# Optimization experiments

Measured on AMD Instinct MI355X. Metric: run time of the kernel, lower is better.

## Reference

```python
import jax, jax.numpy as jnp
import numpy as np

INPUT_LEN = 100000
D_MODEL = 128
NUM_AREAS = 500
NUM_HEADS = 4
DEPTH = D_MODEL // NUM_HEADS          # 32
L = INPUT_LEN // NUM_AREAS            # 200 (per-area length)
MAX_LEN = 2 * (1 + L) - 1             # 401
MASK_NEG = float(np.finfo(np.float16).min) / 10.0  # -6553.6, as in source


def relative_shift(x):
    # x: [B, A, H, L, 2L-1] -> [B, A, H, L, L] (Transformer-XL shift trick)
    B, A, H, t1, m = x.shape
    x = jnp.pad(x, ((0, 0), (0, 0), (0, 0), (0, 0), (1, 0)))  # prepend zero col -> t2 = m+1 = 2L
    t2 = m + 1
    x = x.reshape(B, A, H, t2, t1)
    x = x[:, :, :, 1:, :]
    x = x.reshape(B, A, H, t1, t2 - 1)
    return x[..., : t2 // 2]


def setup_inputs() -> dict:
    key = jax.random.key(0)
    ks = jax.random.split(key, 9)
    s = 0.02
    inp = jax.random.normal(ks[0], (1, INPUT_LEN, D_MODEL), dtype=jnp.float32)
    mask = jax.random.bernoulli(ks[1], 0.1, (1, 1, 1, L, L)).astype(jnp.float32)
    Wq = jax.random.normal(ks[2], (D_MODEL, D_MODEL), dtype=jnp.float32) * s
    Wk = jax.random.normal(ks[3], (D_MODEL, D_MODEL), dtype=jnp.float32) * s
    Wv = jax.random.normal(ks[4], (D_MODEL, D_MODEL), dtype=jnp.float32) * s
    bq = jnp.zeros((D_MODEL,), jnp.float32)
    bk = jnp.zeros((D_MODEL,), jnp.float32)
    bv = jnp.zeros((D_MODEL,), jnp.float32)
    E = jax.random.normal(ks[5], (MAX_LEN, DEPTH), dtype=jnp.float32) * s
    return {"inp": inp, "mask": mask, "Wq": Wq, "bq": bq, "Wk": Wk, "bk": bk,
            "Wv": Wv, "bv": bv, "E": E}


def reference(inp, mask, Wq, bq, Wk, bk, Wv, bv, E):
    B = inp.shape[0]
    x = inp.reshape(B, NUM_AREAS, L, D_MODEL)  # split_areas

    def proj(W, b):
        y = jnp.einsum('bald,de->bale', x, W) + b
        return y.reshape(B, NUM_AREAS, L, NUM_HEADS, DEPTH).transpose(0, 1, 3, 2, 4)

    q = proj(Wq, bq)  # [B, A, H, L, depth]
    k = proj(Wk, bk)
    v = proj(Wv, bv)

    start = max(0, MAX_LEN - (2 * L - 1))  # static = 2
    Eu = E[start:]                          # [2L-1, depth]  (dropout is identity at inference)

    QE = jnp.einsum('bahld,md->bahlm', q, Eu)   # [B, A, H, L, 2L-1]
    Srel = relative_shift(QE)                   # [B, A, H, L, L]
    qk = jnp.einsum('bahld,bahmd->bahlm', q, k) # [B, A, H, L, L]
    logits = (qk + Srel) / jnp.sqrt(jnp.float32(D_MODEL))
    logits = logits + mask * jnp.float32(MASK_NEG)
    attn = jax.nn.softmax(logits, axis=-1)
    out = jnp.einsum('bahlm,bahmd->bahld', attn, v)   # [B, A, H, L, depth]
    out = out.transpose(0, 1, 3, 2, 4).reshape(B, NUM_AREAS, L, D_MODEL)
    return out, attn
```

## Files before the change

### kernel.cpp

```cpp
#include <hip/hip_runtime.h>

typedef short v8s __attribute__((ext_vector_type(8)));
typedef float v4f __attribute__((ext_vector_type(4)));

#define NBH      2000
#define LSEQ     200
#define LPAD     208
#define DEPTH    32
#define DMODEL   128
#define TEU      399
#define MASKNEG  (-6550.4f)
#define QSCALE   0.08838834764831845f

#define BH_ELE   (LPAD * DEPTH)
#define QW_OFF   0
#define KW_OFF   (NBH * BH_ELE)
#define VW_OFF   (2 * NBH * BH_ELE)
#define WT_OFF   (3 * NBH * BH_ELE)
#define EU_OFF   (WT_OFF + 3 * DMODEL * DMODEL)

__device__ __forceinline__ unsigned short f2b(float f) {
  unsigned u = __float_as_uint(f);
  unsigned r = 0x7fffu + ((u >> 16) & 1u);
  return (unsigned short)((u + r) >> 16);
}
__device__ __forceinline__ float b2f(unsigned short u) {
  return __uint_as_float(((unsigned)u) << 16);
}

__global__ void prep_kernel(const float* __restrict__ Wq, const float* __restrict__ Wk,
                            const float* __restrict__ Wv, const float* __restrict__ E,
                            unsigned short* __restrict__ ws) {
  unsigned short* WT = ws + WT_OFF;
  unsigned short* Eu = ws + EU_OFF;
  const int nW = 3 * DMODEL * DMODEL;
  const int total = nW + TEU * DEPTH;
  for (int i = blockIdx.x * blockDim.x + threadIdx.x; i < total; i += gridDim.x * blockDim.x) {
    if (i < nW) {
      int m = i >> 14; int r = i & 16383; int e = r >> 7; int kk = r & 127;
      const float* W = (m == 0) ? Wq : ((m == 1) ? Wk : Wv);
      WT[i] = f2b(W[kk * DMODEL + e]);
    } else {
      int j = i - nW;
      Eu[j] = f2b(E[2 * DEPTH + j]);
    }
  }
}

__global__ __launch_bounds__(256, 4)
void proj_kernel(const float* __restrict__ x, const float* __restrict__ bq,
                 const float* __restrict__ bk, const float* __restrict__ bv,
                 unsigned short* __restrict__ ws) {
  const unsigned short* WT = ws + WT_OFF;
  int bh = blockIdx.x; int a = bh >> 2; int h = bh & 3;
  int tid = threadIdx.x; int wave = tid >> 6; int lane = tid & 63;
  int g = lane >> 4; int c = lane & 15;

  for (int st = wave; st < 13; st += 4) {
    int l0 = st * 16;
    int row = a * LSEQ + min(l0 + c, LSEQ - 1);
    v8s afr[4];
#pragma unroll
    for (int ks = 0; ks < 4; ++ks) {
      const float* p = x + (size_t)row * DMODEL + ks * 32 + 8 * g;
      float4 f0 = *(const float4*)p;
      float4 f1 = *(const float4*)(p + 4);
      v8s t;
      t[0] = (short)f2b(f0.x); t[1] = (short)f2b(f0.y); t[2] = (short)f2b(f0.z); t[3] = (short)f2b(f0.w);
      t[4] = (short)f2b(f1.x); t[5] = (short)f2b(f1.y); t[6] = (short)f2b(f1.z); t[7] = (short)f2b(f1.w);
      afr[ks] = t;
    }
#pragma unroll
    for (int m = 0; m < 3; ++m) {
      const float* bp = (m == 0) ? bq : ((m == 1) ? bk : bv);
#pragma unroll
      for (int nt = 0; nt < 2; ++nt) {
        int col = h * DEPTH + nt * 16 + c;
        v4f acc = {0.f, 0.f, 0.f, 0.f};
#pragma unroll
        for (int ks = 0; ks < 4; ++ks) {
          v8s bfr = *(const v8s*)(WT + ((size_t)(m * DMODEL + col)) * DMODEL + ks * 32 + 8 * g);
          acc = __builtin_amdgcn_mfma_f32_16x16x32_bf16(afr[ks], bfr, acc, 0, 0, 0);
        }
        float bias = bp[col];
        if (m < 2) {
          unsigned short* dst = ws + (m == 0 ? QW_OFF : KW_OFF) + (size_t)bh * BH_ELE
                                + (size_t)l0 * DEPTH + nt * 16 + c;
#pragma unroll
          for (int r = 0; r < 4; ++r) {
            int ll = 4 * g + r;
            float val = acc[r] + bias;
            if (m == 0) val *= QSCALE;
            dst[ll * DEPTH] = (l0 + ll < LSEQ) ? f2b(val) : (unsigned short)0;
          }
        } else {
          ushort4 pk;
          float v0 = acc[0] + bias, v1 = acc[1] + bias, v2 = acc[2] + bias, v3 = acc[3] + bias;
          int lb = l0 + 4 * g;
          pk.x = (lb + 0 < LSEQ) ? f2b(v0) : (unsigned short)0;
          pk.y = (lb + 1 < LSEQ) ? f2b(v1) : (unsigned short)0;
          pk.z = (lb + 2 < LSEQ) ? f2b(v2) : (unsigned short)0;
          pk.w = (lb + 3 < LSEQ) ? f2b(v3) : (unsigned short)0;
          *(ushort4*)(ws + VW_OFF + (size_t)bh * BH_ELE + (size_t)(nt * 16 + c) * LPAD + lb) = pk;
        }
      }
    }
  }
}

__global__ __launch_bounds__(256, 2)
void attn_kernel(const unsigned short* __restrict__ ws, const float* __restrict__ maskp,
                 float* __restrict__ o) {
  __shared__ __align__(16) unsigned short k_lds[LPAD * 40];
  __shared__ __align__(16) unsigned short vT_lds[DEPTH * 216];
  __shared__ __align__(16) unsigned short srel[4][16 * 212];

  int bh = blockIdx.x; int a = bh >> 2; int h = bh & 3;
  int tid = threadIdx.x; int wave = tid >> 6; int lane = tid & 63;
  int g = lane >> 4; int c = lane & 15;

  const unsigned short* qws = ws + QW_OFF + (size_t)bh * BH_ELE;
  const unsigned short* kws = ws + KW_OFF + (size_t)bh * BH_ELE;
  const unsigned short* vws = ws + VW_OFF + (size_t)bh * BH_ELE;
  const unsigned short* eu  = ws + EU_OFF;

  for (int i = tid; i < LPAD * 4; i += 256) {
    int r = i >> 2, cc = i & 3;
    uint4 v = *(const uint4*)(kws + r * 32 + cc * 8);
    *(uint4*)&k_lds[r * 40 + cc * 8] = v;
  }
  for (int i = tid; i < DEPTH * 26; i += 256) {
    int r = i / 26, cc = i - r * 26;
    uint4 v = *(const uint4*)(vws + r * LPAD + cc * 8);
    *(uint4*)&vT_lds[r * 216 + cc * 8] = v;
  }
  __syncthreads();

  float* attn_base = o + 12800000 + (size_t)bh * 40000;
  unsigned short* sw = srel[wave];

  for (int st = wave; st < 13; st += 4) {
    int l0 = st * 16;
    v8s aq = *(const v8s*)(qws + (size_t)(l0 + c) * DEPTH + 8 * g);

    int TB0 = max(0, 184 - l0);
    int ntt = (398 - l0 - TB0 + 16) >> 4;
    for (int tt = 0; tt < ntt; ++tt) {
      int t = TB0 + tt * 16 + c;
      int tc = min(t, 398);
      v8s be = *(const v8s*)(eu + (size_t)tc * DEPTH + 8 * g);
      v4f z = {0.f, 0.f, 0.f, 0.f};
      v4f qe = __builtin_amdgcn_mfma_f32_16x16x32_bf16(aq, be, z, 0, 0, 0);
#pragma unroll
      for (int r = 0; r < 4; ++r) {
        int j = t - 199 + l0 + 4 * g + r;
        if (j >= 0 && j < LSEQ) sw[(4 * g + r) * 212 + j] = f2b(qe[r]);
      }
    }

    v4f S[13];
#pragma unroll
    for (int jt = 0; jt < 13; ++jt) {
      v8s bk_ = *(const v8s*)&k_lds[(jt * 16 + c) * 40 + 8 * g];
      v4f z = {0.f, 0.f, 0.f, 0.f};
      S[jt] = __builtin_amdgcn_mfma_f32_16x16x32_bf16(aq, bk_, z, 0, 0, 0);
    }
#pragma unroll
    for (int jt = 0; jt < 13; ++jt) {
      int j = jt * 16 + c;
      int jc = min(j, LSEQ - 1);
      bool jv = (j < LSEQ);
#pragma unroll
      for (int r = 0; r < 4; ++r) {
        int l = l0 + 4 * g + r;
        float sr = jv ? b2f(sw[(4 * g + r) * 212 + j]) : 0.f;
        float mv = maskp[min(l, LSEQ - 1) * LSEQ + jc];
        S[jt][r] += sr + mv * MASKNEG;
        if (!jv) S[jt][r] = -1e30f;
      }
    }

    float invs[4];
#pragma unroll
    for (int r = 0; r < 4; ++r) {
      float mx = -1e30f;
#pragma unroll
      for (int jt = 0; jt < 13; ++jt) mx = fmaxf(mx, S[jt][r]);
#pragma unroll
      for (int d = 1; d < 16; d <<= 1) mx = fmaxf(mx, __shfl_xor(mx, d, 64));
      float sum = 0.f;
#pragma unroll
      for (int jt = 0; jt < 13; ++jt) { float e = __expf(S[jt][r] - mx); S[jt][r] = e; sum += e; }
#pragma unroll
      for (int d = 1; d < 16; d <<= 1) sum += __shfl_xor(sum, d, 64);
      invs[r] = 1.f / sum;
    }

    v4f oacc0 = {0.f, 0.f, 0.f, 0.f}, oacc1 = {0.f, 0.f, 0.f, 0.f};
#pragma unroll
    for (int jp = 0; jp < 7; ++jp) {
#pragma unroll
      for (int half = 0; half < 2; ++half) {
        int jt = 2 * jp + half;
#pragma unroll
        for (int r = 0; r < 4; ++r) {
          int ll = 4 * g + r;
          float p = 0.f;
          if (jt < 13) {
            p = S[jt][r] * invs[r];
            int l = l0 + ll; int j = jt * 16 + c;
            if (l < LSEQ && j < LSEQ) attn_base[l * LSEQ + j] = p;
          }
          sw[ll * 40 + half * 16 + c] = (jt < 13) ? f2b(p) : (unsigned short)0;
        }
      }
      v8s ap = *(const v8s*)&sw[c * 40 + 8 * g];
      int col0 = min(jp * 32 + 8 * g, 200);
      v8s bv0 = *(const v8s*)&vT_lds[c * 216 + col0];
      v8s bv1 = *(const v8s*)&vT_lds[(16 + c) * 216 + col0];
      oacc0 = __builtin_amdgcn_mfma_f32_16x16x32_bf16(ap, bv0, oacc0, 0, 0, 0);
      oacc1 = __builtin_amdgcn_mfma_f32_16x16x32_bf16(ap, bv1, oacc1, 0, 0, 0);
    }

#pragma unroll
    for (int r = 0; r < 4; ++r) {
      int l = l0 + 4 * g + r;
      if (l < LSEQ) {
        float* op = o + ((size_t)(a * LSEQ + l)) * DMODEL + h * DEPTH;
        op[c] = oacc0[r];
        op[16 + c] = oacc1[r];
      }
    }
  }
}

extern "C" void kernel_launch(void* const* d_in, const int* in_sizes, int n_in,
                              void* d_out, int out_size, void* d_ws, size_t ws_size,
                              hipStream_t stream) {
  const float* inp   = (const float*)d_in[0];
  const float* maskp = (const float*)d_in[1];
  const float* Wq    = (const float*)d_in[2];
  const float* bq    = (const float*)d_in[3];
  const float* Wk    = (const float*)d_in[4];
  const float* bk    = (const float*)d_in[5];
  const float* Wv    = (const float*)d_in[6];
  const float* bv    = (const float*)d_in[7];
  const float* E     = (const float*)d_in[8];
  unsigned short* ws = (unsigned short*)d_ws;
  float* o = (float*)d_out;

  prep_kernel<<<242, 256, 0, stream>>>(Wq, Wk, Wv, E, ws);
  proj_kernel<<<NBH, 256, 0, stream>>>(inp, bq, bk, bv, ws);
  attn_kernel<<<NBH, 256, 0, stream>>>(ws, maskp, o);
}
```

Baseline: 644.6 us.

## Restructure projection per area with LDS-staged bf16 input and V transpose staging

The projection kernel now runs one block per area instead of one per (area, head). It converts the area's input rows to bf16 once into LDS and reuses them across all four heads, which removes the fourfold redundant global reads and conversions of x. V tiles are staged in LDS before being written out transposed, giving coalesced 16-byte stores. In the attention kernel the QE relative-position loop is unrolled into two batches of seven with the E fragments preloaded, to improve load/MFMA overlap. The trade-off is fewer blocks (500), heavier per-block work and extra barriers, plus always computing 14 QE tiles even when fewer are needed.

```diff
diff --git a/kernel.cpp b/kernel.cpp
--- a/kernel.cpp
+++ b/kernel.cpp
@@ -47,64 +47,97 @@
   }
 }
 
-__global__ __launch_bounds__(256, 4)
+__global__ __launch_bounds__(256, 2)
 void proj_kernel(const float* __restrict__ x, const float* __restrict__ bq,
                  const float* __restrict__ bk, const float* __restrict__ bv,
                  unsigned short* __restrict__ ws) {
+  __shared__ __align__(16) unsigned short x_lds[LPAD * 136];
+  __shared__ __align__(16) unsigned short vt_lds[DEPTH * 216];
+
   const unsigned short* WT = ws + WT_OFF;
-  int bh = blockIdx.x; int a = bh >> 2; int h = bh & 3;
+  int a = blockIdx.x;
   int tid = threadIdx.x; int wave = tid >> 6; int lane = tid & 63;
   int g = lane >> 4; int c = lane & 15;
 
-  for (int st = wave; st < 13; st += 4) {
-    int l0 = st * 16;
-    int row = a * LSEQ + min(l0 + c, LSEQ - 1);
-    v8s afr[4];
-#pragma unroll
-    for (int ks = 0; ks < 4; ++ks) {
-      const float* p = x + (size_t)row * DMODEL + ks * 32 + 8 * g;
+  for (int i = tid; i < LPAD * 16; i += 256) {
+    int row = i >> 4; int col = (i & 15) * 8;
+    v8s t = {0, 0, 0, 0, 0, 0, 0, 0};
+    if (row < LSEQ) {
+      const float* p = x + ((size_t)(a * LSEQ + row)) * DMODEL + col;
       float4 f0 = *(const float4*)p;
       float4 f1 = *(const float4*)(p + 4);
-      v8s t;
       t[0] = (short)f2b(f0.x); t[1] = (short)f2b(f0.y); t[2] = (short)f2b(f0.z); t[3] = (short)f2b(f0.w);
       t[4] = (short)f2b(f1.x); t[5] = (short)f2b(f1.y); t[6] = (short)f2b(f1.z); t[7] = (short)f2b(f1.w);
-      afr[ks] = t;
-    }
-#pragma unroll
-    for (int m = 0; m < 3; ++m) {
-      const float* bp = (m == 0) ? bq : ((m == 1) ? bk : bv);
+    }
+    *(v8s*)&x_lds[row * 136 + col] = t;
+  }
+  __syncthreads();
+
+  for (int h = 0; h < 4; ++h) {
+    int bh = a * 4 + h;
+#pragma unroll
+    for (int m = 0; m < 2; ++m) {
+      const float* bp = (m == 0) ? bq : bk;
+      unsigned short* dstbase = ws + (m == 0 ? QW_OFF : KW_OFF) + (size_t)bh * BH_ELE;
 #pragma unroll
       for (int nt = 0; nt < 2; ++nt) {
         int col = h * DEPTH + nt * 16 + c;
-        v4f acc = {0.f, 0.f, 0.f, 0.f};
-#pragma unroll
-        for (int ks = 0; ks < 4; ++ks) {
-          v8s bfr = *(const v8s*)(WT + ((size_t)(m * DMODEL + col)) * DMODEL + ks * 32 + 8 * g);
-          acc = __builtin_amdgcn_mfma_f32_16x16x32_bf16(afr[ks], bfr, acc, 0, 0, 0);
-        }
+        v8s bfr[4];
+#pragma unroll
+        for (int ks = 0; ks < 4; ++ks)
+          bfr[ks] = *(const v8s*)(WT + ((size_t)(m * DMODEL + col)) * DMODEL + ks * 32 + 8 * g);
         float bias = bp[col];
-        if (m < 2) {
-          unsigned short* dst = ws + (m == 0 ? QW_OFF : KW_OFF) + (size_t)bh * BH_ELE
-                                + (size_t)l0 * DEPTH + nt * 16 + c;
+        for (int st = wave; st < 13; st += 4) {
+          int l0 = st * 16;
+          v4f acc = {0.f, 0.f, 0.f, 0.f};
+#pragma unroll
+          for (int ks = 0; ks < 4; ++ks) {
+            v8s afr = *(const v8s*)&x_lds[(l0 + c) * 136 + ks * 32 + 8 * g];
+            acc = __builtin_amdgcn_mfma_f32_16x16x32_bf16(afr, bfr[ks], acc, 0, 0, 0);
+          }
 #pragma unroll
           for (int r = 0; r < 4; ++r) {
             int ll = 4 * g + r;
             float val = acc[r] + bias;
             if (m == 0) val *= QSCALE;
-            dst[ll * DEPTH] = (l0 + ll < LSEQ) ? f2b(val) : (unsigned short)0;
+            dstbase[(size_t)(l0 + ll) * DEPTH + nt * 16 + c] =
+                (l0 + ll < LSEQ) ? f2b(val) : (unsigned short)0;
           }
-        } else {
-          ushort4 pk;
-          float v0 = acc[0] + bias, v1 = acc[1] + bias, v2 = acc[2] + bias, v3 = acc[3] + bias;
-          int lb = l0 + 4 * g;
-          pk.x = (lb + 0 < LSEQ) ? f2b(v0) : (unsigned short)0;
-          pk.y = (lb + 1 < LSEQ) ? f2b(v1) : (unsigned short)0;
-          pk.z = (lb + 2 < LSEQ) ? f2b(v2) : (unsigned short)0;
-          pk.w = (lb + 3 < LSEQ) ? f2b(v3) : (unsigned short)0;
-          *(ushort4*)(ws + VW_OFF + (size_t)bh * BH_ELE + (size_t)(nt * 16 + c) * LPAD + lb) = pk;
         }
       }
     }
+#pragma unroll
+    for (int nt = 0; nt < 2; ++nt) {
+      int col = h * DEPTH + nt * 16 + c;
+      v8s bfr[4];
+#pragma unroll
+      for (int ks = 0; ks < 4; ++ks)
+        bfr[ks] = *(const v8s*)(WT + ((size_t)(2 * DMODEL + col)) * DMODEL + ks * 32 + 8 * g);
+      float bias = bv[col];
+      for (int st = wave; st < 13; st += 4) {
+        int l0 = st * 16;
+        v4f acc = {0.f, 0.f, 0.f, 0.f};
+#pragma unroll
+        for (int ks = 0; ks < 4; ++ks) {
+          v8s afr = *(const v8s*)&x_lds[(l0 + c) * 136 + ks * 32 + 8 * g];
+          acc = __builtin_amdgcn_mfma_f32_16x16x32_bf16(afr, bfr[ks], acc, 0, 0, 0);
+        }
+        ushort4 pk;
+        int lb = l0 + 4 * g;
+        pk.x = (lb + 0 < LSEQ) ? f2b(acc[0] + bias) : (unsigned short)0;
+        pk.y = (lb + 1 < LSEQ) ? f2b(acc[1] + bias) : (unsigned short)0;
+        pk.z = (lb + 2 < LSEQ) ? f2b(acc[2] + bias) : (unsigned short)0;
+        pk.w = (lb + 3 < LSEQ) ? f2b(acc[3] + bias) : (unsigned short)0;
+        *(ushort4*)&vt_lds[(nt * 16 + c) * 216 + lb] = pk;
+      }
+    }
+    __syncthreads();
+    for (int i = tid; i < DEPTH * 26; i += 256) {
+      int r = i / 26, cc = i - r * 26;
+      *(uint4*)(ws + VW_OFF + (size_t)bh * BH_ELE + (size_t)r * LPAD + cc * 8) =
+          *(const uint4*)&vt_lds[r * 216 + cc * 8];
+    }
+    __syncthreads();
   }
 }
 
@@ -118,6 +151,7 @@
   int bh = blockIdx.x; int a = bh >> 2; int h = bh & 3;
   int tid = threadIdx.x; int wave = tid >> 6; int lane = tid & 63;
   int g = lane >> 4; int c = lane & 15;
+  (void)h;
 
   const unsigned short* qws = ws + QW_OFF + (size_t)bh * BH_ELE;
   const unsigned short* kws = ws + KW_OFF + (size_t)bh * BH_ELE;
@@ -131,7 +165,7 @@
   }
   for (int i = tid; i < DEPTH * 26; i += 256) {
     int r = i / 26, cc = i - r * 26;
-    uint4 v = *(const uint4*)(vws + r * LPAD + cc * 8);
+    uint4 v = *(const uint4*)(vws + (size_t)r * LPAD + cc * 8);
     *(uint4*)&vT_lds[r * 216 + cc * 8] = v;
   }
   __syncthreads();
@@ -144,13 +178,29 @@
     v8s aq = *(const v8s*)(qws + (size_t)(l0 + c) * DEPTH + 8 * g);
 
     int TB0 = max(0, 184 - l0);
-    int ntt = (398 - l0 - TB0 + 16) >> 4;
-    for (int tt = 0; tt < ntt; ++tt) {
+    v8s beA[7];
+#pragma unroll
+    for (int tt = 0; tt < 7; ++tt)
+      beA[tt] = *(const v8s*)(eu + (size_t)min(TB0 + tt * 16 + c, 398) * DEPTH + 8 * g);
+#pragma unroll
+    for (int tt = 0; tt < 7; ++tt) {
+      v4f z = {0.f, 0.f, 0.f, 0.f};
+      v4f qe = __builtin_amdgcn_mfma_f32_16x16x32_bf16(aq, beA[tt], z, 0, 0, 0);
       int t = TB0 + tt * 16 + c;
-      int tc = min(t, 398);
-      v8s be = *(const v8s*)(eu + (size_t)tc * DEPTH + 8 * g);
+#pragma unroll
+      for (int r = 0; r < 4; ++r) {
+        int j = t - 199 + l0 + 4 * g + r;
+        if (j >= 0 && j < LSEQ) sw[(4 * g + r) * 212 + j] = f2b(qe[r]);
+      }
+    }
+#pragma unroll
+    for (int tt = 7; tt < 14; ++tt)
+      beA[tt - 7] = *(const v8s*)(eu + (size_t)min(TB0 + tt * 16 + c, 398) * DEPTH + 8 * g);
+#pragma unroll
+    for (int tt = 7; tt < 14; ++tt) {
       v4f z = {0.f, 0.f, 0.f, 0.f};
-      v4f qe = __builtin_amdgcn_mfma_f32_16x16x32_bf16(aq, be, z, 0, 0, 0);
+      v4f qe = __builtin_amdgcn_mfma_f32_16x16x32_bf16(aq, beA[tt - 7], z, 0, 0, 0);
+      int t = TB0 + tt * 16 + c;
 #pragma unroll
       for (int r = 0; r < 4; ++r) {
         int j = t - 199 + l0 + 4 * g + r;
@@ -226,7 +276,7 @@
     for (int r = 0; r < 4; ++r) {
       int l = l0 + 4 * g + r;
       if (l < LSEQ) {
-        float* op = o + ((size_t)(a * LSEQ + l)) * DMODEL + h * DEPTH;
+        float* op = o + ((size_t)(a * LSEQ + l)) * DMODEL + (bh & 3) * DEPTH;
         op[c] = oacc0[r];
         op[16 + c] = oacc1[r];
       }
@@ -250,6 +300,6 @@
   float* o = (float*)d_out;
 
   prep_kernel<<<242, 256, 0, stream>>>(Wq, Wk, Wv, E, ws);
-  proj_kernel<<<NBH, 256, 0, stream>>>(inp, bq, bk, bv, ws);
+  proj_kernel<<<500, 256, 0, stream>>>(inp, bq, bk, bv, ws);
   attn_kernel<<<NBH, 256, 0, stream>>>(ws, maskp, o);
 }
```

Result: faster. 557.5 us (-13.5%).
